# Kernel tuning notes

Measured on AMD Instinct MI355X. Metric: run time of the kernel, lower is better.

The kernel has to match this reference:

```python
import jax, jax.numpy as jnp
import numpy as np

N = 4096; B = 4; NPB = N // B; K = 16
C = 128; COUT = 128; LMAX = 2; L = (LMAX + 1) ** 2  # 9 SH coefficients
H = 8; A = 8; V = 16; HV = H * V
F = 256; NB = 128; FD = 256; CUTOFF = 3.0
E = N * K

def _silu(x):
    return x * jax.nn.sigmoid(x)

def _mish(x):
    return x * jnp.tanh(jax.nn.softplus(x))

def _rms_norm(x, gamma):
    # degree-wise RMS over channel dim, x: [N, L, C]
    s = jnp.sqrt(jnp.mean(x * x, axis=-1, keepdims=True) + 1e-6)
    return x / s * gamma

def _rot_l1(x, R):
    # rotate the l=1 block (coeffs 1:4) of x [E, L, C] by R [E, 3, 3]
    l1 = jnp.einsum('eij,ejc->eic', R, x[:, 1:4, :])
    return jnp.concatenate([x[:, :1, :], l1, x[:, 4:, :]], axis=1)

def _knn(coord, batch):
    d2 = jnp.sum((coord[:, None, :] - coord[None, :, :]) ** 2, axis=-1)  # [N,N]
    same = batch[:, None] == batch[None, :]
    big = jnp.asarray(1e9, d2.dtype)
    d2 = jnp.where(same, d2, big)
    d2 = d2.at[jnp.arange(N), jnp.arange(N)].set(big)
    neg, idx = jax.lax.top_k(-d2, K)
    dist = jnp.sqrt(jnp.maximum(-neg, 0.0))
    edge_src = idx.reshape(-1)                       # [E]
    edge_dst = jnp.repeat(jnp.arange(N), K)          # [E]
    valid = (dist <= CUTOFF).reshape(-1)
    return edge_src, edge_dst, valid

def _edge_rot_mat(edge_vec):
    # deterministic rotation aligning each edge with the y-axis (eSCN-style)
    nx = edge_vec / (jnp.linalg.norm(edge_vec, axis=-1, keepdims=True) + 1e-12)
    ref = jnp.where(jnp.abs(nx[:, :1]) < 0.9,
                    jnp.array([1.0, 0.0, 0.0], nx.dtype),
                    jnp.array([0.0, 1.0, 0.0], nx.dtype))
    nz = jnp.cross(nx, ref)
    nz = nz / (jnp.linalg.norm(nz, axis=-1, keepdims=True) + 1e-12)
    ny = jnp.cross(nz, nx)
    return jnp.stack([nz, nx, ny], axis=1)  # [E,3,3]; R @ edge_dir = e_y

def _forward(node_coord, node_emb, batch, condition,
             W_e1, b_e1, W_e2, b_e2, W_src, W_dst, w_a, W_v, W_o,
             gamma1, gamma2, W_g, W_f1, W_f2, W_film, b_film):
    # dynamic KNN graph; geometry detached as in original (edge_vec.detach())
    coord_g = jax.lax.stop_gradient(node_coord)
    edge_src, edge_dst, valid = _knn(coord_g, batch)
    edge_vec = coord_g[edge_src] - coord_g[edge_dst]                  # [E,3]
    edge_len = jnp.linalg.norm(edge_vec, axis=-1)                     # [E]
    R = _edge_rot_mat(edge_vec)                                       # [E,3,3]
    # gaussian radial basis -> per-edge embedding
    mu = jnp.linspace(0.0, CUTOFF, NB)
    sigma = CUTOFF / NB
    rbf = jnp.exp(-0.5 * ((edge_len[:, None] - mu) / sigma) ** 2)     # [E,NB]
    edge_h = _silu(rbf @ W_e1 + b_e1) @ W_e2 + b_e2                   # [E,HV]
    # equivariant attention (rotate into edge frame, attend, rotate back)
    x_src = _rot_l1(node_emb[edge_src], R)                            # [E,L,C]
    q = node_emb[edge_dst, 0] @ W_dst + x_src[:, 0] @ W_src           # [E,H*A]
    logits = jnp.einsum('eha,ha->eh', _silu(q).reshape(E, H, A), w_a)
    logits = jnp.where(valid[:, None], logits, -1e9)
    m = jax.ops.segment_max(logits, edge_dst, num_segments=N)
    ex = jnp.exp(logits - m[edge_dst])
    den = jax.ops.segment_sum(ex, edge_dst, num_segments=N)
    attn = ex / (den[edge_dst] + 1e-9)                                # [E,H]
    v = jnp.einsum('elc,cv->elv', x_src, W_v) * edge_h[:, None, :]    # [E,L,HV]
    v = v.reshape(E, L, H, V) * attn[:, None, :, None]
    msg = _rot_l1(v.reshape(E, L, HV), jnp.swapaxes(R, 1, 2))         # back to global frame
    agg = jax.ops.segment_sum(msg, edge_dst, num_segments=N)          # [N,L,HV]
    x = node_emb + jnp.einsum('nlv,vc->nlc', agg, W_o)
    # FFN with separable S2 (scalar-gated) activation
    h = _rms_norm(x, gamma2)
    gate = _silu(h[:, 0] @ W_g)                                       # [N,F]
    hid = jnp.einsum('nlc,cf->nlf', h, W_f1) * gate[:, None, :]
    x = x + jnp.einsum('nlf,fo->nlo', hid, W_f2)
    x = _rms_norm(x, gamma1)
    # FiLM conditioning over flattened (L*C) per batch element
    film = _mish(condition) @ W_film + b_film                         # [B, 2*L*COUT]
    w, bfi = film[:, :L * COUT], film[:, L * COUT:]
    c = x.reshape(B, NPB, L * COUT) * w[:, None, :] + bfi[:, None, :]
    return c.reshape(N, L, COUT)

def setup_inputs():
    key = jax.random.key(0)
    ks = jax.random.split(key, 16)
    node_coord = jax.random.uniform(ks[0], (N, 3)) * 2.0
    node_emb = jax.random.normal(ks[1], (N, L, C)) * 0.1
    batch = jnp.arange(N, dtype=jnp.int64 if jax.config.jax_enable_x64 else jnp.int32) // NPB
    condition = jax.random.normal(ks[2], (B, FD))
    s = lambda d: 1.0 / np.sqrt(d)
    return {
        'node_coord': node_coord, 'node_emb': node_emb, 'batch': batch, 'condition': condition,
        'W_e1': jax.random.normal(ks[3], (NB, 128)) * s(NB), 'b_e1': jnp.zeros((128,)),
        'W_e2': jax.random.normal(ks[4], (128, HV)) * s(128), 'b_e2': jnp.zeros((HV,)),
        'W_src': jax.random.normal(ks[5], (C, H * A)) * s(C),
        'W_dst': jax.random.normal(ks[6], (C, H * A)) * s(C),
        'w_a': jax.random.normal(ks[7], (H, A)) * s(A),
        'W_v': jax.random.normal(ks[8], (C, HV)) * s(C),
        'W_o': jax.random.normal(ks[9], (HV, C)) * s(HV),
        'gamma1': jnp.ones((C,)), 'gamma2': jnp.ones((C,)),
        'W_g': jax.random.normal(ks[10], (C, F)) * s(C),
        'W_f1': jax.random.normal(ks[11], (C, F)) * s(C),
        'W_f2': jax.random.normal(ks[12], (F, COUT)) * s(F),
        'W_film': jax.random.normal(ks[13], (FD, 2 * L * COUT)) * s(FD),
        'b_film': jnp.zeros((2 * L * COUT,)),
    }

def reference(node_coord, node_emb, batch, condition,
              W_e1, b_e1, W_e2, b_e2, W_src, W_dst, w_a, W_v, W_o,
              gamma1, gamma2, W_g, W_f1, W_f2, W_film, b_film):
    out = _forward(node_coord, node_emb, batch, condition,
                   W_e1, b_e1, W_e2, b_e2, W_src, W_dst, w_a, W_v, W_o,
                   gamma1, gamma2, W_g, W_f1, W_f2, W_film, b_film)
    return (node_coord, out, batch)
```

## Files before the change

### kernel.cpp

```cpp
#include <hip/hip_runtime.h>

#define NNODE 4096
#define NPB   1024

__device__ __forceinline__ float siluf(float x){ return x / (1.0f + expf(-x)); }

__global__ __launch_bounds__(256) void k_film(const float* __restrict__ cond,
                                              const float* __restrict__ Wfilm,
                                              const float* __restrict__ bfilm,
                                              float* __restrict__ filmG){
  __shared__ float mL[256];
  int b = blockIdx.y;
  int t = threadIdx.x;
  int j = blockIdx.x*256 + t;
  float x = cond[b*256 + t];
  float sp = fmaxf(x, 0.f) + log1pf(expf(-fabsf(x)));
  mL[t] = x * tanhf(sp);
  __syncthreads();
  if(j >= 2304) return;
  float acc = bfilm[j];
  for(int i=0;i<256;i++) acc += mL[i] * Wfilm[i*2304 + j];
  filmG[b*2304 + j] = acc;
}

__global__ __launch_bounds__(256) void k_pre(const float* __restrict__ emb,
                                             const float* __restrict__ Wv,
                                             const float* __restrict__ Wsrc,
                                             const float* __restrict__ Wdst,
                                             float* __restrict__ ZG,
                                             float* __restrict__ QsG,
                                             float* __restrict__ QdG){
  const int t = threadIdx.x;
  const int rg = __builtin_amdgcn_readfirstlane(t >> 6);
  const int lane = t & 63;
  const int c0 = lane*2;
  const int n = blockIdx.x*4 + rg;
  const float* en = emb + (size_t)n*1152;

  float z[9][2];
  #pragma unroll
  for(int l=0;l<9;l++){ z[l][0]=0.f; z[l][1]=0.f; }
  for(int c4=0;c4<32;c4++){
    float2 wv0 = *(const float2*)&Wv[(c4*4+0)*128 + c0];
    float2 wv1 = *(const float2*)&Wv[(c4*4+1)*128 + c0];
    float2 wv2 = *(const float2*)&Wv[(c4*4+2)*128 + c0];
    float2 wv3 = *(const float2*)&Wv[(c4*4+3)*128 + c0];
    #pragma unroll
    for(int l=0;l<9;l++){
      float4 x4 = *(const float4*)&en[l*128 + c4*4];
      z[l][0] += x4.x*wv0.x + x4.y*wv1.x + x4.z*wv2.x + x4.w*wv3.x;
      z[l][1] += x4.x*wv0.y + x4.y*wv1.y + x4.z*wv2.y + x4.w*wv3.y;
    }
  }
  #pragma unroll
  for(int l=0;l<9;l++){
    float2 o; o.x=z[l][0]; o.y=z[l][1];
    *(float2*)&ZG[(size_t)n*1152 + l*128 + c0] = o;
  }
  float qs = 0.f, qd = 0.f;
  for(int c=0;c<128;c++){
    float ec = en[c];
    qs = fmaf(ec, Wsrc[c*64 + lane], qs);
    qd = fmaf(ec, Wdst[c*64 + lane], qd);
  }
  QsG[n*64 + lane] = qs;
  QdG[n*64 + lane] = qd;
}

#define E2_HD   0
#define E2_RB   2048
#define E2_AT   2304
#define E2_KI   2432
#define E2_LEN  2448
#define E2_VL   2464
#define E2_W0   2480
#define E2_NPF  2560
__global__ __launch_bounds__(128) void k_edge(
    const float* __restrict__ coord,
    const float* __restrict__ We1, const float* __restrict__ be1,
    const float* __restrict__ We2, const float* __restrict__ be2,
    const float* __restrict__ wa,
    const float* __restrict__ Qs, const float* __restrict__ Qd,
    const float* __restrict__ Z,
    float* __restrict__ out){
  __shared__ __align__(16) float S[2*E2_NPF];
  int* Si = (int*)S;
  const int t = threadIdx.x;
  const int w = __builtin_amdgcn_readfirstlane(t >> 6);
  const int lane = t & 63;
  const int n = blockIdx.x*2 + w;
  const int base = n & ~(NPB - 1);
  const int self = n - base;
  const int NP = w * E2_NPF;
  const int c0 = lane*2;
  const int myh = lane >> 3;
  float* aggG = out + 12288;

  {
    const float* cb = coord + (size_t)base*3;
    const float cx = cb[self*3+0];
    const float cy = cb[self*3+1];
    const float cz = cb[self*3+2];
    float d2a[16]; int ida[16];
    #pragma unroll
    for(int q=0;q<16;q++){
      int j = lane + q*64;
      float dx = __fsub_rn(cb[j*3+0], cx);
      float dy = __fsub_rn(cb[j*3+1], cy);
      float dz = __fsub_rn(cb[j*3+2], cz);
      float d2 = __fadd_rn(__fadd_rn(__fmul_rn(dx,dx), __fmul_rn(dy,dy)), __fmul_rn(dz,dz));
      if(j == self) d2 = 3e38f;
      d2a[q] = d2; ida[q] = j;
    }
    for(int r=0;r<16;r++){
      float bd = d2a[0]; int bi = ida[0];
      #pragma unroll
      for(int q=1;q<16;q++){
        bool bet = (d2a[q] < bd) || (d2a[q] == bd && ida[q] < bi);
        if(bet){ bd = d2a[q]; bi = ida[q]; }
      }
      for(int s=1;s<64;s<<=1){
        float od = __shfl_xor(bd, s, 64);
        int   oi = __shfl_xor(bi, s, 64);
        bool bet = (od < bd) || (od == bd && oi < bi);
        if(bet){ bd = od; bi = oi; }
      }
      if(lane == 0){
        Si[NP + E2_KI + r] = bi;
        float len = __fsqrt_rn(bd);
        S[NP + E2_LEN + r] = len;
        S[NP + E2_VL + r]  = (len <= 3.0f) ? 1.0f : 0.0f;
        int i0 = (int)(len * (127.0f/3.0f) + 0.5f);
        int w0 = i0 - 7;
        w0 = w0 < 0 ? 0 : (w0 > 112 ? 112 : w0);
        Si[NP + E2_W0 + r] = w0;
      }
      #pragma unroll
      for(int q=0;q<16;q++) if(ida[q] == bi) d2a[q] = 3e38f;
    }
  }
  __syncthreads();

  {
    const int e0 = lane >> 3, hh = lane & 7;
    float4 qda = *(const float4*)&Qd[(size_t)n*64 + hh*8];
    float4 qdb = *(const float4*)&Qd[(size_t)n*64 + hh*8 + 4];
    float4 waa = *(const float4*)&wa[hh*8];
    float4 wab = *(const float4*)&wa[hh*8 + 4];
    float lg[2];
    #pragma unroll
    for(int s=0;s<2;s++){
      int e = e0 + s*8;
      int src = base + Si[NP + E2_KI + e];
      float4 qa = *(const float4*)&Qs[(size_t)src*64 + hh*8];
      float4 qb = *(const float4*)&Qs[(size_t)src*64 + hh*8 + 4];
      float sv = siluf(qda.x+qa.x)*waa.x + siluf(qda.y+qa.y)*waa.y
               + siluf(qda.z+qa.z)*waa.z + siluf(qda.w+qa.w)*waa.w
               + siluf(qdb.x+qb.x)*wab.x + siluf(qdb.y+qb.y)*wab.y
               + siluf(qdb.z+qb.z)*wab.z + siluf(qdb.w+qb.w)*wab.w;
      lg[s] = (S[NP + E2_VL + e] > 0.5f) ? sv : -1e9f;
    }
    float m = fmaxf(lg[0], lg[1]);
    m = fmaxf(m, __shfl_xor(m, 8, 64));
    m = fmaxf(m, __shfl_xor(m, 16, 64));
    m = fmaxf(m, __shfl_xor(m, 32, 64));
    float ex0 = expf(lg[0] - m), ex1 = expf(lg[1] - m);
    float den = ex0 + ex1;
    den += __shfl_xor(den, 8, 64);
    den += __shfl_xor(den, 16, 64);
    den += __shfl_xor(den, 32, 64);
    float inv = 1.0f/(den + 1e-9f);
    S[NP + E2_AT + lane]      = ex0*inv;
    S[NP + E2_AT + 64 + lane] = ex1*inv;

    const float step = 3.0f/127.0f;
    const float sigma = 3.0f/128.0f;
    #pragma unroll
    for(int k=0;k<4;k++){
      int idx = lane + k*64;
      int e = idx >> 4, wi = idx & 15;
      float len = S[NP + E2_LEN + e];
      int bin = Si[NP + E2_W0 + e] + wi;
      float d = (len - step*(float)bin) / sigma;
      S[NP + E2_RB + idx] = expf(-0.5f*d*d);
    }
  }
  __syncthreads();

  {
    float a4[16][2]; int b0e[16];
    #pragma unroll
    for(int e=0;e<16;e++){ a4[e][0]=0.f; a4[e][1]=0.f; b0e[e] = Si[NP + E2_W0 + e]; }
    for(int wi=0; wi<16; wi++){
      #pragma unroll
      for(int e=0;e<16;e++){
        float rb = S[NP + E2_RB + e*16 + wi];
        float2 we = *(const float2*)&We1[(size_t)(b0e[e] + wi)*128 + c0];
        a4[e][0] = fmaf(rb, we.x, a4[e][0]);
        a4[e][1] = fmaf(rb, we.y, a4[e][1]);
      }
    }
    float2 b1v = *(const float2*)&be1[c0];
    #pragma unroll
    for(int e=0;e<16;e++){
      float2 o; o.x = siluf(a4[e][0] + b1v.x); o.y = siluf(a4[e][1] + b1v.y);
      *(float2*)&S[NP + E2_HD + e*128 + c0] = o;
    }
  }
  __syncthreads();

  float a5[16][2];
  #pragma unroll
  for(int e=0;e<16;e++){ a5[e][0]=0.f; a5[e][1]=0.f; }
  for(int c4=0;c4<32;c4++){
    float2 w0 = *(const float2*)&We2[(c4*4+0)*128 + c0];
    float2 w1 = *(const float2*)&We2[(c4*4+1)*128 + c0];
    float2 w2 = *(const float2*)&We2[(c4*4+2)*128 + c0];
    float2 w3 = *(const float2*)&We2[(c4*4+3)*128 + c0];
    #pragma unroll
    for(int e=0;e<16;e++){
      float4 h4 = *(const float4*)&S[NP + E2_HD + e*128 + c4*4];
      a5[e][0] += h4.x*w0.x + h4.y*w1.x + h4.z*w2.x + h4.w*w3.x;
      a5[e][1] += h4.x*w0.y + h4.y*w1.y + h4.z*w2.y + h4.w*w3.y;
    }
  }

  {
    float2 b2v = *(const float2*)&be2[c0];
    float ag[9][2];
    #pragma unroll
    for(int l=0;l<9;l++){ ag[l][0]=0.f; ag[l][1]=0.f; }
    #pragma unroll
    for(int e=0;e<16;e++){
      int src = base + Si[NP + E2_KI + e];
      const float* zp = &Z[(size_t)src*1152 + c0];
      float at = S[NP + E2_AT + e*8 + myh];
      float sc0 = (a5[e][0] + b2v.x) * at;
      float sc1 = (a5[e][1] + b2v.y) * at;
      #pragma unroll
      for(int l=0;l<9;l++){
        float2 z2 = *(const float2*)&zp[l*128];
        ag[l][0] = fmaf(z2.x, sc0, ag[l][0]);
        ag[l][1] = fmaf(z2.y, sc1, ag[l][1]);
      }
    }
    #pragma unroll
    for(int l=0;l<9;l++){
      float2 o; o.x = ag[l][0]; o.y = ag[l][1];
      *(float2*)&aggG[(size_t)n*1152 + l*128 + c0] = o;
    }
  }
}

#define FW_ACT 0
#define FW_HID 1152
#define FW_SZ  2304
__global__ __launch_bounds__(256) void k_ffn(
    const float* __restrict__ emb,
    const float* __restrict__ Wo,
    const float* __restrict__ g1, const float* __restrict__ g2,
    const float* __restrict__ Wg, const float* __restrict__ Wf1,
    const float* __restrict__ Wf2,
    const float* __restrict__ filmG,
    float* __restrict__ out){
  __shared__ __align__(16) float S[4*FW_SZ];
  const int t = threadIdx.x;
  const int rg = __builtin_amdgcn_readfirstlane(t >> 6);
  const int u2 = t & 63;
  const int c0 = u2*2;
  const int n = blockIdx.x*4 + rg;
  float* W_ = &S[rg*FW_SZ];
  float* aggG = out + 12288;
  const float* agp = aggG + (size_t)n*1152;

  float x[9][2];
  #pragma unroll
  for(int l=0;l<9;l++){ x[l][0]=0.f; x[l][1]=0.f; }
  for(int c4=0;c4<32;c4++){
    float2 w0 = *(const float2*)&Wo[(c4*4+0)*128 + c0];
    float2 w1 = *(const float2*)&Wo[(c4*4+1)*128 + c0];
    float2 w2 = *(const float2*)&Wo[(c4*4+2)*128 + c0];
    float2 w3 = *(const float2*)&Wo[(c4*4+3)*128 + c0];
    #pragma unroll
    for(int l=0;l<9;l++){
      float4 a4 = *(const float4*)&agp[l*128 + c4*4];
      x[l][0] += a4.x*w0.x + a4.y*w1.x + a4.z*w2.x + a4.w*w3.x;
      x[l][1] += a4.x*w0.y + a4.y*w1.y + a4.z*w2.y + a4.w*w3.y;
    }
  }

  float g2a = g2[c0], g2b = g2[c0+1];
  #pragma unroll
  for(int l=0;l<9;l++){
    float2 e2 = *(const float2*)&emb[(size_t)n*1152 + l*128 + c0];
    x[l][0] += e2.x; x[l][1] += e2.y;
    float sq = x[l][0]*x[l][0] + x[l][1]*x[l][1];
    #pragma unroll
    for(int s=1;s<64;s<<=1) sq += __shfl_xor(sq, s, 64);
    float ss = sqrtf(sq/128.f + 1e-6f);
    float2 o; o.x = x[l][0]/ss*g2a; o.y = x[l][1]/ss*g2b;
    *(float2*)&W_[FW_ACT + l*128 + c0] = o;
  }

  float ha[2][9][2]; float ga[2][2];
  #pragma unroll
  for(int ft=0;ft<2;ft++){
    ga[ft][0]=0.f; ga[ft][1]=0.f;
    #pragma unroll
    for(int l=0;l<9;l++){ ha[ft][l][0]=0.f; ha[ft][l][1]=0.f; }
  }
  for(int c4=0;c4<32;c4++){
    float2 wf[2][4], wg_[2][4];
    #pragma unroll
    for(int ft=0;ft<2;ft++)
      #pragma unroll
      for(int i=0;i<4;i++){
        wf[ft][i]  = *(const float2*)&Wf1[(c4*4+i)*256 + ft*128 + c0];
        wg_[ft][i] = *(const float2*)&Wg [(c4*4+i)*256 + ft*128 + c0];
      }
    float4 h0 = *(const float4*)&W_[FW_ACT + 0*128 + c4*4];
    #pragma unroll
    for(int ft=0;ft<2;ft++){
      ga[ft][0] += h0.x*wg_[ft][0].x + h0.y*wg_[ft][1].x + h0.z*wg_[ft][2].x + h0.w*wg_[ft][3].x;
      ga[ft][1] += h0.x*wg_[ft][0].y + h0.y*wg_[ft][1].y + h0.z*wg_[ft][2].y + h0.w*wg_[ft][3].y;
      ha[ft][0][0] += h0.x*wf[ft][0].x + h0.y*wf[ft][1].x + h0.z*wf[ft][2].x + h0.w*wf[ft][3].x;
      ha[ft][0][1] += h0.x*wf[ft][0].y + h0.y*wf[ft][1].y + h0.z*wf[ft][2].y + h0.w*wf[ft][3].y;
    }
    #pragma unroll
    for(int l=1;l<9;l++){
      float4 h4 = *(const float4*)&W_[FW_ACT + l*128 + c4*4];
      #pragma unroll
      for(int ft=0;ft<2;ft++){
        ha[ft][l][0] += h4.x*wf[ft][0].x + h4.y*wf[ft][1].x + h4.z*wf[ft][2].x + h4.w*wf[ft][3].x;
        ha[ft][l][1] += h4.x*wf[ft][0].y + h4.y*wf[ft][1].y + h4.z*wf[ft][2].y + h4.w*wf[ft][3].y;
      }
    }
  }

  #pragma unroll
  for(int ft=0;ft<2;ft++){
    float gx = siluf(ga[ft][0]), gy = siluf(ga[ft][1]);
    #pragma unroll
    for(int l=0;l<9;l++){
      float2 o; o.x = ha[ft][l][0]*gx; o.y = ha[ft][l][1]*gy;
      *(float2*)&W_[FW_HID + l*128 + c0] = o;
    }
    for(int f4=0;f4<32;f4++){
      float2 w0 = *(const float2*)&Wf2[(ft*128 + f4*4+0)*128 + c0];
      float2 w1 = *(const float2*)&Wf2[(ft*128 + f4*4+1)*128 + c0];
      float2 w2 = *(const float2*)&Wf2[(ft*128 + f4*4+2)*128 + c0];
      float2 w3 = *(const float2*)&Wf2[(ft*128 + f4*4+3)*128 + c0];
      #pragma unroll
      for(int l=0;l<9;l++){
        float4 h4 = *(const float4*)&W_[FW_HID + l*128 + f4*4];
        x[l][0] += h4.x*w0.x + h4.y*w1.x + h4.z*w2.x + h4.w*w3.x;
        x[l][1] += h4.x*w0.y + h4.y*w1.y + h4.z*w2.y + h4.w*w3.y;
      }
    }
  }

  {
    float g1a = g1[c0], g1b = g1[c0+1];
    int b = n >> 10;
    #pragma unroll
    for(int l=0;l<9;l++){
      float sq = x[l][0]*x[l][0] + x[l][1]*x[l][1];
      #pragma unroll
      for(int s=1;s<64;s<<=1) sq += __shfl_xor(sq, s, 64);
      float ss = sqrtf(sq/128.f + 1e-6f);
      float2 fw = *(const float2*)&filmG[b*2304 + l*128 + c0];
      float2 fb = *(const float2*)&filmG[b*2304 + 1152 + l*128 + c0];
      float2 o;
      o.x = x[l][0]/ss*g1a*fw.x + fb.x;
      o.y = x[l][1]/ss*g1b*fw.y + fb.y;
      *(float2*)&out[12288 + (size_t)n*1152 + l*128 + c0] = o;
    }
  }
}

__global__ __launch_bounds__(256) void k_copy(const float* __restrict__ coord,
                                              float* __restrict__ out){
  int i = blockIdx.x*256 + threadIdx.x;
  if(i < 12288) out[i] = coord[i];
  int n = i - 12288;
  if(n >= 0 && n < 4096) out[12288 + 4718592 + n] = (float)(n >> 10);
}

extern "C" void kernel_launch(void* const* d_in, const int* in_sizes, int n_in,
                              void* d_out, int out_size, void* d_ws, size_t ws_size,
                              hipStream_t stream) {
  const float* coord = (const float*)d_in[0];
  const float* emb   = (const float*)d_in[1];
  const float* cond  = (const float*)d_in[3];
  const float* We1   = (const float*)d_in[4];
  const float* be1   = (const float*)d_in[5];
  const float* We2   = (const float*)d_in[6];
  const float* be2   = (const float*)d_in[7];
  const float* Wsrc  = (const float*)d_in[8];
  const float* Wdst  = (const float*)d_in[9];
  const float* wa    = (const float*)d_in[10];
  const float* Wv    = (const float*)d_in[11];
  const float* Wo    = (const float*)d_in[12];
  const float* g1    = (const float*)d_in[13];
  const float* g2    = (const float*)d_in[14];
  const float* Wg    = (const float*)d_in[15];
  const float* Wf1   = (const float*)d_in[16];
  const float* Wf2   = (const float*)d_in[17];
  const float* Wfilm = (const float*)d_in[18];
  const float* bfilm = (const float*)d_in[19];

  float* outf  = (float*)d_out;
  float* filmG = (float*)d_ws;
  float* QsG   = filmG + 9216;
  float* QdG   = QsG + 262144;
  float* ZG    = QdG + 262144;

  k_film<<<dim3(9,4), 256, 0, stream>>>(cond, Wfilm, bfilm, filmG);
  k_pre<<<NNODE/4, 256, 0, stream>>>(emb, Wv, Wsrc, Wdst, ZG, QsG, QdG);
  k_edge<<<NNODE/2, 128, 0, stream>>>(coord, We1, be1, We2, be2, wa,
                                      QsG, QdG, ZG, outf);
  k_ffn<<<NNODE/4, 256, 0, stream>>>(emb, Wo, g1, g2, Wg, Wf1, Wf2,
                                     filmG, outf);
  k_copy<<<64, 256, 0, stream>>>(coord, outf);
}
```

Before: 410.6 us.

## Fuse edge aggregation and node FFN into one per-node kernel

Merges the edge-aggregation kernel and the FFN kernel into a single kernel. The aggregated messages stay in shared memory instead of round-tripping through a global buffer. This removes one launch and the global write and read of the [N,9,128] aggregate. In exchange the fused kernel runs two nodes per 128-thread block instead of four per 256, and holds more registers, which may lower occupancy for the FFN part.

```diff
diff --git a/kernel.cpp b/kernel.cpp
--- a/kernel.cpp
+++ b/kernel.cpp
@@ -74,14 +74,22 @@
 #define E2_LEN  2448
 #define E2_VL   2464
 #define E2_W0   2480
+#define F_ACT   0
+#define F_HID   1152
 #define E2_NPF  2560
-__global__ __launch_bounds__(128) void k_edge(
+__global__ __launch_bounds__(128) void k_node(
     const float* __restrict__ coord,
+    const float* __restrict__ emb,
     const float* __restrict__ We1, const float* __restrict__ be1,
     const float* __restrict__ We2, const float* __restrict__ be2,
     const float* __restrict__ wa,
+    const float* __restrict__ Wo,
+    const float* __restrict__ g1, const float* __restrict__ g2,
+    const float* __restrict__ Wg, const float* __restrict__ Wf1,
+    const float* __restrict__ Wf2,
     const float* __restrict__ Qs, const float* __restrict__ Qd,
     const float* __restrict__ Z,
+    const float* __restrict__ filmG,
     float* __restrict__ out){
   __shared__ __align__(16) float S[2*E2_NPF];
   int* Si = (int*)S;
@@ -94,7 +102,6 @@
   const int NP = w * E2_NPF;
   const int c0 = lane*2;
   const int myh = lane >> 3;
-  float* aggG = out + 12288;
 
   {
     const float* cb = coord + (size_t)base*3;
@@ -247,31 +254,11 @@
     #pragma unroll
     for(int l=0;l<9;l++){
       float2 o; o.x = ag[l][0]; o.y = ag[l][1];
-      *(float2*)&aggG[(size_t)n*1152 + l*128 + c0] = o;
-    }
-  }
-}
-
-#define FW_ACT 0
-#define FW_HID 1152
-#define FW_SZ  2304
-__global__ __launch_bounds__(256) void k_ffn(
-    const float* __restrict__ emb,
-    const float* __restrict__ Wo,
-    const float* __restrict__ g1, const float* __restrict__ g2,
-    const float* __restrict__ Wg, const float* __restrict__ Wf1,
-    const float* __restrict__ Wf2,
-    const float* __restrict__ filmG,
-    float* __restrict__ out){
-  __shared__ __align__(16) float S[4*FW_SZ];
-  const int t = threadIdx.x;
-  const int rg = __builtin_amdgcn_readfirstlane(t >> 6);
-  const int u2 = t & 63;
-  const int c0 = u2*2;
-  const int n = blockIdx.x*4 + rg;
-  float* W_ = &S[rg*FW_SZ];
-  float* aggG = out + 12288;
-  const float* agp = aggG + (size_t)n*1152;
+      *(float2*)&S[NP + F_ACT + l*128 + c0] = o;
+    }
+  }
+
+  float* W_ = &S[NP];
 
   float x[9][2];
   #pragma unroll
@@ -283,23 +270,25 @@
     float2 w3 = *(const float2*)&Wo[(c4*4+3)*128 + c0];
     #pragma unroll
     for(int l=0;l<9;l++){
-      float4 a4 = *(const float4*)&agp[l*128 + c4*4];
+      float4 a4 = *(const float4*)&W_[F_ACT + l*128 + c4*4];
       x[l][0] += a4.x*w0.x + a4.y*w1.x + a4.z*w2.x + a4.w*w3.x;
       x[l][1] += a4.x*w0.y + a4.y*w1.y + a4.z*w2.y + a4.w*w3.y;
     }
   }
 
-  float g2a = g2[c0], g2b = g2[c0+1];
-  #pragma unroll
-  for(int l=0;l<9;l++){
-    float2 e2 = *(const float2*)&emb[(size_t)n*1152 + l*128 + c0];
-    x[l][0] += e2.x; x[l][1] += e2.y;
-    float sq = x[l][0]*x[l][0] + x[l][1]*x[l][1];
-    #pragma unroll
-    for(int s=1;s<64;s<<=1) sq += __shfl_xor(sq, s, 64);
-    float ss = sqrtf(sq/128.f + 1e-6f);
-    float2 o; o.x = x[l][0]/ss*g2a; o.y = x[l][1]/ss*g2b;
-    *(float2*)&W_[FW_ACT + l*128 + c0] = o;
+  {
+    float g2a = g2[c0], g2b = g2[c0+1];
+    #pragma unroll
+    for(int l=0;l<9;l++){
+      float2 e2 = *(const float2*)&emb[(size_t)n*1152 + l*128 + c0];
+      x[l][0] += e2.x; x[l][1] += e2.y;
+      float sq = x[l][0]*x[l][0] + x[l][1]*x[l][1];
+      #pragma unroll
+      for(int s=1;s<64;s<<=1) sq += __shfl_xor(sq, s, 64);
+      float ss = sqrtf(sq/128.f + 1e-6f);
+      float2 o; o.x = x[l][0]/ss*g2a; o.y = x[l][1]/ss*g2b;
+      *(float2*)&W_[F_ACT + l*128 + c0] = o;
+    }
   }
 
   float ha[2][9][2]; float ga[2][2];
@@ -318,7 +307,7 @@
         wf[ft][i]  = *(const float2*)&Wf1[(c4*4+i)*256 + ft*128 + c0];
         wg_[ft][i] = *(const float2*)&Wg [(c4*4+i)*256 + ft*128 + c0];
       }
-    float4 h0 = *(const float4*)&W_[FW_ACT + 0*128 + c4*4];
+    float4 h0 = *(const float4*)&W_[F_ACT + 0*128 + c4*4];
     #pragma unroll
     for(int ft=0;ft<2;ft++){
       ga[ft][0] += h0.x*wg_[ft][0].x + h0.y*wg_[ft][1].x + h0.z*wg_[ft][2].x + h0.w*wg_[ft][3].x;
@@ -328,7 +317,7 @@
     }
     #pragma unroll
     for(int l=1;l<9;l++){
-      float4 h4 = *(const float4*)&W_[FW_ACT + l*128 + c4*4];
+      float4 h4 = *(const float4*)&W_[F_ACT + l*128 + c4*4];
       #pragma unroll
       for(int ft=0;ft<2;ft++){
         ha[ft][l][0] += h4.x*wf[ft][0].x + h4.y*wf[ft][1].x + h4.z*wf[ft][2].x + h4.w*wf[ft][3].x;
@@ -343,7 +332,7 @@
     #pragma unroll
     for(int l=0;l<9;l++){
       float2 o; o.x = ha[ft][l][0]*gx; o.y = ha[ft][l][1]*gy;
-      *(float2*)&W_[FW_HID + l*128 + c0] = o;
+      *(float2*)&W_[F_HID + l*128 + c0] = o;
     }
     for(int f4=0;f4<32;f4++){
       float2 w0 = *(const float2*)&Wf2[(ft*128 + f4*4+0)*128 + c0];
@@ -352,7 +341,7 @@
       float2 w3 = *(const float2*)&Wf2[(ft*128 + f4*4+3)*128 + c0];
       #pragma unroll
       for(int l=0;l<9;l++){
-        float4 h4 = *(const float4*)&W_[FW_HID + l*128 + f4*4];
+        float4 h4 = *(const float4*)&W_[F_HID + l*128 + f4*4];
         x[l][0] += h4.x*w0.x + h4.y*w1.x + h4.z*w2.x + h4.w*w3.x;
         x[l][1] += h4.x*w0.y + h4.y*w1.y + h4.z*w2.y + h4.w*w3.y;
       }
@@ -417,9 +406,9 @@
 
   k_film<<<dim3(9,4), 256, 0, stream>>>(cond, Wfilm, bfilm, filmG);
   k_pre<<<NNODE/4, 256, 0, stream>>>(emb, Wv, Wsrc, Wdst, ZG, QsG, QdG);
-  k_edge<<<NNODE/2, 128, 0, stream>>>(coord, We1, be1, We2, be2, wa,
-                                      QsG, QdG, ZG, outf);
-  k_ffn<<<NNODE/4, 256, 0, stream>>>(emb, Wo, g1, g2, Wg, Wf1, Wf2,
-                                     filmG, outf);
+  k_node<<<NNODE/2, 128, 0, stream>>>(coord, emb,
+                                      We1, be1, We2, be2, wa,
+                                      Wo, g1, g2, Wg, Wf1, Wf2,
+                                      QsG, QdG, ZG, filmG, outf);
   k_copy<<<64, 256, 0, stream>>>(coord, outf);
 }
```

Result: slower. 462.5 us (+12.6%).
